# Kernel optimization log

Hardware: AMD Instinct MI355X
Metric: run time of the kernel (lower is better)

Reference implementation:

```python
import jax, jax.numpy as jnp
import numpy as np

B, S, E, D, M = 512, 64, 768, 256, 3  # batch, seq, encoder_dim, dim, num_modalities


def setup_inputs() -> dict:
    key = jax.random.key(0)
    ks = jax.random.split(key, 16)
    inp = {}
    for i in range(M):
        inp[f"latent{i}"] = jax.random.normal(ks[i], (B, S, E), dtype=jnp.float32)
        inp[f"Wp{i}"] = jax.random.normal(ks[3 + i], (D, E), dtype=jnp.float32) * (1.0 / np.sqrt(E))
        inp[f"bp{i}"] = jnp.zeros((D,), dtype=jnp.float32)
    inp["corr"] = jax.random.uniform(ks[7], (D, D), dtype=jnp.float32, minval=-0.1, maxval=0.1)
    F_in = 2 * D * (M - 1)  # 1024
    inp["Wb"] = jax.random.normal(ks[8], (64, F_in), dtype=jnp.float32) * (1.0 / np.sqrt(F_in))
    inp["bb"] = jnp.zeros((64,), dtype=jnp.float32)
    inp["gamma"] = jnp.ones((64,), dtype=jnp.float32)
    inp["beta"] = jnp.zeros((64,), dtype=jnp.float32)
    return inp


def _forward(latents, Wps, bps, corr, Wb, bb, gamma, beta):
    # project each modality: [B,S,E] -> [B,S,D]
    proj = [lat @ Wp.T + bp for lat, Wp, bp in zip(latents, Wps, bps)]
    anchor = proj[0]
    pairs = []
    for other in proj[1:]:
        # cc[b,i,j] = anchor[b,i,:] @ corr @ other[b,j,:]
        cc = jnp.einsum('bid,de,bje->bij', anchor, corr, other)
        a_att = jax.nn.softmax(cc, axis=1)   # softmax over anchor tokens
        o_att = jax.nn.softmax(cc, axis=2)   # softmax over other tokens (= softmax(cc^T, dim=1))
        att_anchor = jnp.einsum('bid,bij->bdj', anchor, a_att) + jnp.swapaxes(anchor, 1, 2)
        att_other = jnp.einsum('bjd,bij->bdi', other, o_att) + jnp.swapaxes(other, 1, 2)
        pairs.append(jnp.concatenate([att_anchor, att_other], axis=1))  # [B,2D,S]
    fused = jnp.concatenate(pairs, axis=1)          # [B, 2D(M-1), S]
    fused = jnp.swapaxes(fused, 1, 2)               # [B, S, 2D(M-1)]
    h = fused @ Wb.T + bb                           # [B, S, 64]
    mu = jnp.mean(h, axis=-1, keepdims=True)
    var = jnp.var(h, axis=-1, keepdims=True)
    h = (h - mu) / jnp.sqrt(var + 1e-5) * gamma + beta
    return jax.nn.relu(h)


def reference(latent0, latent1, latent2, Wp0, bp0, Wp1, bp1, Wp2, bp2, corr, Wb, bb, gamma, beta):
    return _forward([latent0, latent1, latent2], [Wp0, Wp1, Wp2], [bp0, bp1, bp2],
                    corr, Wb, bb, gamma, beta)
```

## Files before the change

### kernel.cpp

```cpp
#include <hip/hip_runtime.h>
#include <hip/hip_bf16.h>
#include <stdint.h>

#define Bsz 512
#define Ssz 64
#define Esz 768
#define Dsz 256
#define MROWS (Bsz * Ssz)
#define FIN 1024

typedef _Float16 f16;
typedef f16 f16x4 __attribute__((ext_vector_type(4)));
typedef f16 f16x8v __attribute__((ext_vector_type(8)));
typedef float f32x4 __attribute__((ext_vector_type(4)));

__device__ __forceinline__ void async_copy16(const void* g, void* l) {
    __builtin_amdgcn_global_load_lds((const __attribute__((address_space(1))) uint32_t*)g,
                                     (__attribute__((address_space(3))) uint32_t*)l, 16, 0, 0);
}

__global__ __launch_bounds__(256) void prep(const float* __restrict__ Wp0,
                                            const float* __restrict__ Wp1,
                                            const float* __restrict__ Wp2,
                                            const float* __restrict__ corr,
                                            const float* __restrict__ Wb,
                                            f16* __restrict__ Wph,
                                            f16* __restrict__ corrT,
                                            f16* __restrict__ Wbh) {
    const int t = blockIdx.x * 256 + threadIdx.x;
    if (t < 3 * 196608) {
        const int z = t / 196608, i = t % 196608;
        const float* W = (z == 0) ? Wp0 : (z == 1) ? Wp1 : Wp2;
        Wph[(size_t)z * 196608 + i] = (f16)W[i];
    }
    if (t < 65536) {
        const int d = t >> 8, e = t & 255;
        corrT[e * 256 + d] = (f16)corr[d * 256 + e];
        Wbh[t] = (f16)Wb[t];
    }
}

template <bool A_F16, bool BIAS>
__global__ __launch_bounds__(256) void mfma_gemm(
    const float* __restrict__ A32a, const float* __restrict__ A32b,
    const float* __restrict__ A32c, const f16* __restrict__ A16,
    const f16* __restrict__ Bh, const float* __restrict__ biasA,
    const float* __restrict__ biasB, const float* __restrict__ biasC,
    f16* __restrict__ Ch, int K) {
    constexpr int LDS_BYTES = A_F16 ? 32768 : 49152;
    __shared__ __align__(16) char smem[LDS_BYTES];
    float* Af32 = (float*)smem;
    f16* Af16 = (f16*)smem;
    f16* Bf = (f16*)(smem + (A_F16 ? 16384 : 32768));
    f16* Ce = (f16*)smem;

    const int tid = threadIdx.x;
    const int n0 = blockIdx.x * 128;
    const int m0 = blockIdx.y * 128;
    const int z = blockIdx.z;
    const float* A32 = (z == 0) ? A32a : (z == 1) ? A32b : A32c;
    const float* bias = (z == 0) ? biasA : (z == 1) ? biasB : biasC;
    const f16* Bz = Bh + (size_t)z * 256 * K;
    f16* Cz = Ch + (size_t)z * MROWS * 256;

    const int lane = tid & 63;
    const int w = tid >> 6;
    const int lr = lane & 15;
    const int lk = lane >> 4;
    const int ma = (w >> 1) * 4;
    const int nb = (w & 1) * 4;

    f32x4 acc[4][4];
#pragma unroll
    for (int i = 0; i < 4; i++)
#pragma unroll
        for (int j = 0; j < 4; j++) acc[i][j] = (f32x4){0.f, 0.f, 0.f, 0.f};

    for (int k0 = 0; k0 < K; k0 += 64) {
        __syncthreads();
#pragma unroll
        for (int i = 0; i < (A_F16 ? 4 : 8); i++) {
            const int Ub = (w * (A_F16 ? 4 : 8) + i) * 64;
            const int U = Ub + lane;
            if constexpr (A_F16) {
                const int row = U >> 3, u = (U & 7) ^ (row & 7);
                async_copy16(A16 + (size_t)(m0 + row) * K + k0 + u * 8, Af16 + (size_t)Ub * 8);
            } else {
                const int row = U >> 4, c = (U & 15) ^ (row & 15);
                async_copy16(A32 + (size_t)(m0 + row) * K + k0 + c * 4, Af32 + (size_t)Ub * 4);
            }
        }
#pragma unroll
        for (int i = 0; i < 4; i++) {
            const int Ub = (w * 4 + i) * 64;
            const int U = Ub + lane;
            const int row = U >> 3, u = (U & 7) ^ (row & 7);
            async_copy16(Bz + (size_t)(n0 + row) * K + k0 + u * 8, Bf + (size_t)Ub * 8);
        }
        __syncthreads();
#pragma unroll
        for (int kh = 0; kh < 2; kh++) {
            f16x8v af[4], bf[4];
#pragma unroll
            for (int i = 0; i < 4; i++) {
                const int row = (ma + i) * 16 + lr;
                if constexpr (A_F16) {
                    const int u = (kh * 4 + lk) ^ (row & 7);
                    af[i] = *(const f16x8v*)&Af16[(row * 8 + u) * 8];
                } else {
                    const int c = kh * 8 + lk * 2;
                    const float4 v1 = *(const float4*)&Af32[(row * 16 + (c ^ lr)) * 4];
                    const float4 v2 = *(const float4*)&Af32[(row * 16 + ((c + 1) ^ lr)) * 4];
                    f16x8v h;
                    h[0] = (f16)v1.x; h[1] = (f16)v1.y; h[2] = (f16)v1.z; h[3] = (f16)v1.w;
                    h[4] = (f16)v2.x; h[5] = (f16)v2.y; h[6] = (f16)v2.z; h[7] = (f16)v2.w;
                    af[i] = h;
                }
            }
#pragma unroll
            for (int j = 0; j < 4; j++) {
                const int row = (nb + j) * 16 + lr;
                const int u = (kh * 4 + lk) ^ (row & 7);
                bf[j] = *(const f16x8v*)&Bf[(row * 8 + u) * 8];
            }
#pragma unroll
            for (int i = 0; i < 4; i++)
#pragma unroll
                for (int j = 0; j < 4; j++)
                    acc[i][j] = __builtin_amdgcn_mfma_f32_16x16x32_f16(af[i], bf[j], acc[i][j], 0, 0, 0);
        }
    }

    __syncthreads();
    const int cr = lane & 15, qr = lane >> 4;
    const int mwl = (w >> 1) * 64;
    const int nwl = (w & 1) * 64;
#pragma unroll
    for (int i = 0; i < 4; i++) {
#pragma unroll
        for (int j = 0; j < 4; j++) {
            const int col = nwl + j * 16 + cr;
            const float bv = BIAS ? bias[n0 + col] : 0.f;
#pragma unroll
            for (int r = 0; r < 4; r++) {
                const int row = mwl + i * 16 + qr * 4 + r;
                Ce[row * 128 + col] = (f16)(acc[i][j][r] + bv);
            }
        }
    }
    __syncthreads();
#pragma unroll
    for (int r = 0; r < 8; r++) {
        const int f = r * 256 + tid;
        const int row = f >> 4, c16 = f & 15;
        uint4 v = *(const uint4*)&Ce[row * 128 + c16 * 8];
        *(uint4*)(Cz + (size_t)(m0 + row) * 256 + n0 + c16 * 8) = v;
    }
}

__global__ __launch_bounds__(256) void cc_softmax(const f16* __restrict__ ac,
                                                  const f16* __restrict__ proj1,
                                                  const f16* __restrict__ proj2,
                                                  f16* __restrict__ aT,
                                                  f16* __restrict__ oP) {
    const int b = blockIdx.x, q = blockIdx.y;
    const f16* __restrict__ A = ac + (size_t)b * Ssz * Dsz;
    const f16* __restrict__ Bp = (q ? proj2 : proj1) + (size_t)b * Ssz * Dsz;
    __shared__ float sc[64][65];
    __shared__ float cmax[64], csum[64], rmax[64], rsum[64];
    const int tid = threadIdx.x;
    const int lane = tid & 63, w = tid >> 6;
    const int lr = lane & 15;
    const int lk = lane >> 4;

    f32x4 acc[4];
#pragma unroll
    for (int j = 0; j < 4; j++) acc[j] = (f32x4){0.f, 0.f, 0.f, 0.f};

    const f16* __restrict__ Arow = A + (size_t)(w * 16 + lr) * Dsz + lk * 8;
    for (int ks = 0; ks < 8; ks++) {
        f16x8v af = *(const f16x8v*)(Arow + ks * 32);
        f16x8v bf[4];
#pragma unroll
        for (int j = 0; j < 4; j++)
            bf[j] = *(const f16x8v*)(Bp + (size_t)(j * 16 + lr) * Dsz + ks * 32 + lk * 8);
#pragma unroll
        for (int j = 0; j < 4; j++)
            acc[j] = __builtin_amdgcn_mfma_f32_16x16x32_f16(af, bf[j], acc[j], 0, 0, 0);
    }
#pragma unroll
    for (int j = 0; j < 4; j++)
#pragma unroll
        for (int r = 0; r < 4; r++) sc[w * 16 + lk * 4 + r][j * 16 + lr] = acc[j][r];
    __syncthreads();
    if (tid < 64) {
        const int j = tid;
        float m = -1e30f;
        for (int i = 0; i < 64; i++) m = fmaxf(m, sc[i][j]);
        float s = 0.f;
        for (int i = 0; i < 64; i++) s += __expf(sc[i][j] - m);
        cmax[j] = m;
        csum[j] = s;
    } else if (tid < 128) {
        const int i = tid - 64;
        float m = -1e30f;
        for (int j = 0; j < 64; j++) m = fmaxf(m, sc[i][j]);
        float s = 0.f;
        for (int j = 0; j < 64; j++) s += __expf(sc[i][j] - m);
        rmax[i] = m;
        rsum[i] = s;
    }
    __syncthreads();
    const int lid = tid & 63;
    const int grp = tid >> 6;
    f16* __restrict__ apT = aT + (size_t)(q * Bsz + b) * 4096;
    f16* __restrict__ opR = oP + (size_t)(q * Bsz + b) * 4096;
    for (int i = grp; i < 64; i += 4) {
        const float v = __expf(sc[i][lid] - rmax[i]) / rsum[i];
        opR[i * 64 + lid] = (f16)v;
    }
    for (int jj = grp; jj < 64; jj += 4) {
        const float v = __expf(sc[lid][jj] - cmax[jj]) / csum[jj];
        apT[jj * 64 + lid] = (f16)v;
    }
}

__global__ __launch_bounds__(256) void g_gemm(const f16* __restrict__ proj,
                                              const f16* __restrict__ Wbh,
                                              f16* __restrict__ G) {
    const int b = blockIdx.x;
    const int tid = threadIdx.x, lane = tid & 63, w = tid >> 6;
    const int q = w >> 1, part = w & 1;
    const int z = part ? (1 + q) : 0;
    const f16* __restrict__ X = proj + ((size_t)z * MROWS + b * 64) * 256;
    const f16* __restrict__ Wc = Wbh + q * 512 + part * 256;
    const int lr = lane & 15, lk = lane >> 4;

    f32x4 acc[4][4];
#pragma unroll
    for (int i = 0; i < 4; i++)
#pragma unroll
        for (int j = 0; j < 4; j++) acc[i][j] = (f32x4){0.f, 0.f, 0.f, 0.f};

    for (int ks = 0; ks < 8; ks++) {
        f16x8v af[4], bf[4];
#pragma unroll
        for (int mi = 0; mi < 4; mi++)
            af[mi] = *(const f16x8v*)(Wc + (size_t)(mi * 16 + lr) * FIN + ks * 32 + lk * 8);
#pragma unroll
        for (int nj = 0; nj < 4; nj++)
            bf[nj] = *(const f16x8v*)(X + (size_t)(nj * 16 + lr) * 256 + ks * 32 + lk * 8);
#pragma unroll
        for (int mi = 0; mi < 4; mi++)
#pragma unroll
            for (int nj = 0; nj < 4; nj++)
                acc[mi][nj] = __builtin_amdgcn_mfma_f32_16x16x32_f16(af[mi], bf[nj], acc[mi][nj], 0, 0, 0);
    }

    __shared__ __align__(16) f16 Gs[4][4096];
#pragma unroll
    for (int mi = 0; mi < 4; mi++)
#pragma unroll
        for (int nj = 0; nj < 4; nj++)
#pragma unroll
            for (int r = 0; r < 4; r++)
                Gs[w][(mi * 16 + lk * 4 + r) * 64 + nj * 16 + lr] = (f16)acc[mi][nj][r];
    __syncthreads();
#pragma unroll
    for (int r = 0; r < 8; r++) {
        const int u = r * 64 + lane;
        *(uint4*)(G + ((size_t)(b * 4 + w)) * 4096 + u * 8) = *(const uint4*)&Gs[w][u * 8];
    }
}

__global__ __launch_bounds__(256) void attn_ln(const f16* __restrict__ aT,
                                               const f16* __restrict__ oP,
                                               const f16* __restrict__ G,
                                               const float* __restrict__ bb,
                                               const float* __restrict__ gamma,
                                               const float* __restrict__ beta,
                                               float* __restrict__ out) {
    const int b = blockIdx.x;
    const int tid = threadIdx.x, lane = tid & 63, w = tid >> 6;
    const int lr = lane & 15, lk = lane >> 4;

    __shared__ __align__(16) f16 Gs[4][4096];
#pragma unroll
    for (int r = 0; r < 8; r++) {
        const int gu = r * 256 + tid;
        const int term = gu >> 9, u = gu & 511;
        const int o = u >> 3, tch = u & 7;
        uint4 v = *(const uint4*)(G + ((size_t)(b * 4 + term)) * 4096 + u * 8);
        const int su = o * 8 + (tch ^ (o & 7));
        *(uint4*)&Gs[term][su * 8] = v;
    }
    __syncthreads();

    f32x4 acc[4];
#pragma unroll
    for (int j = 0; j < 4; j++) acc[j] = (f32x4){0.f, 0.f, 0.f, 0.f};

#pragma unroll
    for (int term = 0; term < 4; term++) {
        const int q = term >> 1;
        const f16* __restrict__ Abase =
            ((term & 1) ? oP : aT) + ((size_t)(q * Bsz + b)) * 4096;
#pragma unroll
        for (int kh = 0; kh < 2; kh++) {
            f16x8v af = *(const f16x8v*)(Abase + (size_t)(w * 16 + lr) * 64 + kh * 32 + lk * 8);
#pragma unroll
            for (int jf = 0; jf < 4; jf++) {
                const int o = jf * 16 + lr;
                const int su = o * 8 + ((kh * 4 + lk) ^ (o & 7));
                f16x8v bf = *(const f16x8v*)&Gs[term][su * 8];
                acc[jf] = __builtin_amdgcn_mfma_f32_16x16x32_f16(af, bf, acc[jf], 0, 0, 0);
            }
        }
    }

    float bbv[4], gv[4], bv2[4];
#pragma unroll
    for (int jf = 0; jf < 4; jf++) {
        const int o = jf * 16 + lr;
        bbv[jf] = bb[o];
        gv[jf] = gamma[o];
        bv2[jf] = beta[o];
    }
#pragma unroll
    for (int r = 0; r < 4; r++) {
        const int s = w * 16 + lk * 4 + r;
        float h[4];
        float s1 = 0.f, s2 = 0.f;
#pragma unroll
        for (int jf = 0; jf < 4; jf++) {
            const int o = jf * 16 + lr;
            float resid = 0.f;
#pragma unroll
            for (int term = 0; term < 4; term++) {
                const int su = o * 8 + ((s >> 3) ^ (o & 7));
                resid += (float)Gs[term][su * 8 + (s & 7)];
            }
            h[jf] = acc[jf][r] + resid + bbv[jf];
            s1 += h[jf];
            s2 += h[jf] * h[jf];
        }
#pragma unroll
        for (int m = 1; m < 16; m <<= 1) {
            s1 += __shfl_xor(s1, m);
            s2 += __shfl_xor(s2, m);
        }
        const float mu = s1 * (1.f / 64.f);
        const float inv = rsqrtf(s2 * (1.f / 64.f) - mu * mu + 1e-5f);
#pragma unroll
        for (int jf = 0; jf < 4; jf++) {
            const float v = (h[jf] - mu) * inv * gv[jf] + bv2[jf];
            out[(size_t)(b * 64 + s) * 64 + jf * 16 + lr] = fmaxf(v, 0.f);
        }
    }
}

extern "C" void kernel_launch(void* const* d_in, const int* in_sizes, int n_in,
                              void* d_out, int out_size, void* d_ws, size_t ws_size,
                              hipStream_t stream) {
    const float* latent0 = (const float*)d_in[0];
    const float* Wp0 = (const float*)d_in[1];
    const float* bp0 = (const float*)d_in[2];
    const float* latent1 = (const float*)d_in[3];
    const float* Wp1 = (const float*)d_in[4];
    const float* bp1 = (const float*)d_in[5];
    const float* latent2 = (const float*)d_in[6];
    const float* Wp2 = (const float*)d_in[7];
    const float* bp2 = (const float*)d_in[8];
    const float* corr = (const float*)d_in[9];
    const float* Wb = (const float*)d_in[10];
    const float* bb = (const float*)d_in[11];
    const float* gamma = (const float*)d_in[12];
    const float* beta = (const float*)d_in[13];

    char* ws = (char*)d_ws;
    f16* proj_h = (f16*)ws;
    f16* ac_h = (f16*)(ws + 48ull * 1024 * 1024);
    f16* aT = (f16*)(ws + 64ull * 1024 * 1024);
    f16* oP = (f16*)(ws + 72ull * 1024 * 1024);
    f16* G = (f16*)(ws + 80ull * 1024 * 1024);
    f16* Wph = (f16*)(ws + 160ull * 1024 * 1024);
    f16* corrT = (f16*)(ws + 162ull * 1024 * 1024);
    f16* Wbh = (f16*)(ws + 162ull * 1024 * 1024 + 128ull * 1024);

    float* out = (float*)d_out;
    dim3 blk(256);

    prep<<<2304, blk, 0, stream>>>(Wp0, Wp1, Wp2, corr, Wb, Wph, corrT, Wbh);

    mfma_gemm<false, true><<<dim3(2, 256, 3), blk, 0, stream>>>(
        latent0, latent1, latent2, (const f16*)nullptr, Wph, bp0, bp1, bp2, proj_h, Esz);

    mfma_gemm<true, false><<<dim3(2, 256, 1), blk, 0, stream>>>(
        (const float*)nullptr, (const float*)nullptr, (const float*)nullptr, proj_h,
        corrT, (const float*)nullptr, (const float*)nullptr, (const float*)nullptr,
        ac_h, Dsz);

    const f16* proj1_h = proj_h + (size_t)MROWS * 256;
    const f16* proj2_h = proj_h + 2ull * MROWS * 256;

    cc_softmax<<<dim3(Bsz, 2), blk, 0, stream>>>(ac_h, proj1_h, proj2_h, aT, oP);

    g_gemm<<<Bsz, blk, 0, stream>>>(proj_h, Wbh, G);

    attn_ln<<<Bsz, blk, 0, stream>>>(aT, oP, G, bb, gamma, beta, out);

    (void)in_sizes; (void)n_in; (void)out_size; (void)ws_size;
}
```

Measured before the change: 396.6 us.

## Double-buffer GEMM loads, parallelize softmax stats, fuse G GEMM into tail

The projection GEMM now double-buffers its LDS tiles, issuing async loads for the next K slice while it computes on the current one, so each iteration waits on one barrier instead of two. The cc_softmax statistics are spread across all 256 threads using partial max and sum followed by a merge, replacing the old setup where only 128 threads did serial 64-element scans. The g_gemm kernel is folded into the attention/layernorm tail, which drops one launch and the round trip of G through global memory. In exchange, the GEMM uses twice as much LDS (96KB for the f32 variant), which can cut occupancy.

```diff
diff --git a/kernel.cpp b/kernel.cpp
--- a/kernel.cpp
+++ b/kernel.cpp
@@ -47,12 +47,9 @@
     const f16* __restrict__ Bh, const float* __restrict__ biasA,
     const float* __restrict__ biasB, const float* __restrict__ biasC,
     f16* __restrict__ Ch, int K) {
-    constexpr int LDS_BYTES = A_F16 ? 32768 : 49152;
-    __shared__ __align__(16) char smem[LDS_BYTES];
-    float* Af32 = (float*)smem;
-    f16* Af16 = (f16*)smem;
-    f16* Bf = (f16*)(smem + (A_F16 ? 16384 : 32768));
-    f16* Ce = (f16*)smem;
+    constexpr int ABYTES = A_F16 ? 16384 : 32768;
+    constexpr int BUF = ABYTES + 16384;
+    __shared__ __align__(16) char smem[2 * BUF];
 
     const int tid = threadIdx.x;
     const int n0 = blockIdx.x * 128;
@@ -76,18 +73,18 @@
 #pragma unroll
         for (int j = 0; j < 4; j++) acc[i][j] = (f32x4){0.f, 0.f, 0.f, 0.f};
 
-    for (int k0 = 0; k0 < K; k0 += 64) {
-        __syncthreads();
+    auto stage = [&](int buf, int k0) {
+        char* base = smem + buf * BUF;
 #pragma unroll
         for (int i = 0; i < (A_F16 ? 4 : 8); i++) {
             const int Ub = (w * (A_F16 ? 4 : 8) + i) * 64;
             const int U = Ub + lane;
             if constexpr (A_F16) {
                 const int row = U >> 3, u = (U & 7) ^ (row & 7);
-                async_copy16(A16 + (size_t)(m0 + row) * K + k0 + u * 8, Af16 + (size_t)Ub * 8);
+                async_copy16(A16 + (size_t)(m0 + row) * K + k0 + u * 8, base + Ub * 16);
             } else {
                 const int row = U >> 4, c = (U & 15) ^ (row & 15);
-                async_copy16(A32 + (size_t)(m0 + row) * K + k0 + c * 4, Af32 + (size_t)Ub * 4);
+                async_copy16(A32 + (size_t)(m0 + row) * K + k0 + c * 4, base + Ub * 16);
             }
         }
 #pragma unroll
@@ -95,9 +92,21 @@
             const int Ub = (w * 4 + i) * 64;
             const int U = Ub + lane;
             const int row = U >> 3, u = (U & 7) ^ (row & 7);
-            async_copy16(Bz + (size_t)(n0 + row) * K + k0 + u * 8, Bf + (size_t)Ub * 8);
-        }
-        __syncthreads();
+            async_copy16(Bz + (size_t)(n0 + row) * K + k0 + u * 8, base + ABYTES + Ub * 16);
+        }
+    };
+
+    stage(0, 0);
+    __syncthreads();
+    int cur = 0;
+    const int NT = K >> 6;
+    for (int t = 0; t < NT; t++) {
+        if (t + 1 < NT) stage(cur ^ 1, (t + 1) << 6);
+        __builtin_amdgcn_sched_barrier(0);
+        const char* base = smem + cur * BUF;
+        const f16* Af16L = (const f16*)base;
+        const float* Af32L = (const float*)base;
+        const f16* BfL = (const f16*)(base + ABYTES);
 #pragma unroll
         for (int kh = 0; kh < 2; kh++) {
             f16x8v af[4], bf[4];
@@ -106,11 +115,11 @@
                 const int row = (ma + i) * 16 + lr;
                 if constexpr (A_F16) {
                     const int u = (kh * 4 + lk) ^ (row & 7);
-                    af[i] = *(const f16x8v*)&Af16[(row * 8 + u) * 8];
+                    af[i] = *(const f16x8v*)&Af16L[(row * 8 + u) * 8];
                 } else {
                     const int c = kh * 8 + lk * 2;
-                    const float4 v1 = *(const float4*)&Af32[(row * 16 + (c ^ lr)) * 4];
-                    const float4 v2 = *(const float4*)&Af32[(row * 16 + ((c + 1) ^ lr)) * 4];
+                    const float4 v1 = *(const float4*)&Af32L[(row * 16 + (c ^ lr)) * 4];
+                    const float4 v2 = *(const float4*)&Af32L[(row * 16 + ((c + 1) ^ lr)) * 4];
                     f16x8v h;
                     h[0] = (f16)v1.x; h[1] = (f16)v1.y; h[2] = (f16)v1.z; h[3] = (f16)v1.w;
                     h[4] = (f16)v2.x; h[5] = (f16)v2.y; h[6] = (f16)v2.z; h[7] = (f16)v2.w;
@@ -121,7 +130,7 @@
             for (int j = 0; j < 4; j++) {
                 const int row = (nb + j) * 16 + lr;
                 const int u = (kh * 4 + lk) ^ (row & 7);
-                bf[j] = *(const f16x8v*)&Bf[(row * 8 + u) * 8];
+                bf[j] = *(const f16x8v*)&BfL[(row * 8 + u) * 8];
             }
 #pragma unroll
             for (int i = 0; i < 4; i++)
@@ -129,9 +138,11 @@
                 for (int j = 0; j < 4; j++)
                     acc[i][j] = __builtin_amdgcn_mfma_f32_16x16x32_f16(af[i], bf[j], acc[i][j], 0, 0, 0);
         }
-    }
-
-    __syncthreads();
+        __syncthreads();
+        cur ^= 1;
+    }
+
+    f16* Ce = (f16*)smem;
     const int cr = lane & 15, qr = lane >> 4;
     const int mwl = (w >> 1) * 64;
     const int nwl = (w & 1) * 64;
@@ -167,7 +178,8 @@
     const f16* __restrict__ A = ac + (size_t)b * Ssz * Dsz;
     const f16* __restrict__ Bp = (q ? proj2 : proj1) + (size_t)b * Ssz * Dsz;
     __shared__ float sc[64][65];
-    __shared__ float cmax[64], csum[64], rmax[64], rsum[64];
+    __shared__ float pm[4][64], ps[4][64], qm[4][64], qs[4][64];
+    __shared__ float CM[64], CI[64], RM[64], RI[64];
     const int tid = threadIdx.x;
     const int lane = tid & 63, w = tid >> 6;
     const int lr = lane & 15;
@@ -193,106 +205,95 @@
 #pragma unroll
         for (int r = 0; r < 4; r++) sc[w * 16 + lk * 4 + r][j * 16 + lr] = acc[j][r];
     __syncthreads();
-    if (tid < 64) {
-        const int j = tid;
-        float m = -1e30f;
-        for (int i = 0; i < 64; i++) m = fmaxf(m, sc[i][j]);
-        float s = 0.f;
-        for (int i = 0; i < 64; i++) s += __expf(sc[i][j] - m);
-        cmax[j] = m;
-        csum[j] = s;
-    } else if (tid < 128) {
-        const int i = tid - 64;
-        float m = -1e30f;
-        for (int j = 0; j < 64; j++) m = fmaxf(m, sc[i][j]);
-        float s = 0.f;
-        for (int j = 0; j < 64; j++) s += __expf(sc[i][j] - m);
-        rmax[i] = m;
-        rsum[i] = s;
-    }
-    __syncthreads();
-    const int lid = tid & 63;
-    const int grp = tid >> 6;
+
+    const int lid = tid & 63, qa = tid >> 6;
+    float m1 = -1e30f, m2 = -1e30f;
+#pragma unroll
+    for (int it = 0; it < 16; it++) {
+        m1 = fmaxf(m1, sc[qa * 16 + it][lid]);
+        m2 = fmaxf(m2, sc[lid][qa * 16 + it]);
+    }
+    float s1 = 0.f, s2 = 0.f;
+#pragma unroll
+    for (int it = 0; it < 16; it++) {
+        s1 += __expf(sc[qa * 16 + it][lid] - m1);
+        s2 += __expf(sc[lid][qa * 16 + it] - m2);
+    }
+    pm[qa][lid] = m1; ps[qa][lid] = s1;
+    qm[qa][lid] = m2; qs[qa][lid] = s2;
+    __syncthreads();
+    if (tid < 128) {
+        const int x = tid & 63;
+        const bool col = tid < 64;
+        float M = -1e30f;
+#pragma unroll
+        for (int u = 0; u < 4; u++) M = fmaxf(M, col ? pm[u][x] : qm[u][x]);
+        float S = 0.f;
+#pragma unroll
+        for (int u = 0; u < 4; u++)
+            S += (col ? ps[u][x] : qs[u][x]) * __expf((col ? pm[u][x] : qm[u][x]) - M);
+        if (col) { CM[x] = M; CI[x] = 1.f / S; }
+        else     { RM[x] = M; RI[x] = 1.f / S; }
+    }
+    __syncthreads();
     f16* __restrict__ apT = aT + (size_t)(q * Bsz + b) * 4096;
     f16* __restrict__ opR = oP + (size_t)(q * Bsz + b) * 4096;
-    for (int i = grp; i < 64; i += 4) {
-        const float v = __expf(sc[i][lid] - rmax[i]) / rsum[i];
-        opR[i * 64 + lid] = (f16)v;
-    }
-    for (int jj = grp; jj < 64; jj += 4) {
-        const float v = __expf(sc[lid][jj] - cmax[jj]) / csum[jj];
-        apT[jj * 64 + lid] = (f16)v;
-    }
-}
-
-__global__ __launch_bounds__(256) void g_gemm(const f16* __restrict__ proj,
-                                              const f16* __restrict__ Wbh,
-                                              f16* __restrict__ G) {
-    const int b = blockIdx.x;
-    const int tid = threadIdx.x, lane = tid & 63, w = tid >> 6;
-    const int q = w >> 1, part = w & 1;
-    const int z = part ? (1 + q) : 0;
-    const f16* __restrict__ X = proj + ((size_t)z * MROWS + b * 64) * 256;
-    const f16* __restrict__ Wc = Wbh + q * 512 + part * 256;
-    const int lr = lane & 15, lk = lane >> 4;
-
-    f32x4 acc[4][4];
-#pragma unroll
-    for (int i = 0; i < 4; i++)
-#pragma unroll
-        for (int j = 0; j < 4; j++) acc[i][j] = (f32x4){0.f, 0.f, 0.f, 0.f};
-
-    for (int ks = 0; ks < 8; ks++) {
-        f16x8v af[4], bf[4];
-#pragma unroll
-        for (int mi = 0; mi < 4; mi++)
-            af[mi] = *(const f16x8v*)(Wc + (size_t)(mi * 16 + lr) * FIN + ks * 32 + lk * 8);
-#pragma unroll
-        for (int nj = 0; nj < 4; nj++)
-            bf[nj] = *(const f16x8v*)(X + (size_t)(nj * 16 + lr) * 256 + ks * 32 + lk * 8);
-#pragma unroll
-        for (int mi = 0; mi < 4; mi++)
-#pragma unroll
-            for (int nj = 0; nj < 4; nj++)
-                acc[mi][nj] = __builtin_amdgcn_mfma_f32_16x16x32_f16(af[mi], bf[nj], acc[mi][nj], 0, 0, 0);
-    }
-
-    __shared__ __align__(16) f16 Gs[4][4096];
-#pragma unroll
-    for (int mi = 0; mi < 4; mi++)
-#pragma unroll
-        for (int nj = 0; nj < 4; nj++)
-#pragma unroll
-            for (int r = 0; r < 4; r++)
-                Gs[w][(mi * 16 + lk * 4 + r) * 64 + nj * 16 + lr] = (f16)acc[mi][nj][r];
-    __syncthreads();
-#pragma unroll
-    for (int r = 0; r < 8; r++) {
-        const int u = r * 64 + lane;
-        *(uint4*)(G + ((size_t)(b * 4 + w)) * 4096 + u * 8) = *(const uint4*)&Gs[w][u * 8];
-    }
-}
-
-__global__ __launch_bounds__(256) void attn_ln(const f16* __restrict__ aT,
-                                               const f16* __restrict__ oP,
-                                               const f16* __restrict__ G,
-                                               const float* __restrict__ bb,
-                                               const float* __restrict__ gamma,
-                                               const float* __restrict__ beta,
-                                               float* __restrict__ out) {
+#pragma unroll
+    for (int it = 0; it < 16; it++) {
+        const int i = qa * 16 + it;
+        opR[i * 64 + lid] = (f16)(__expf(sc[i][lid] - RM[i]) * RI[i]);
+        apT[i * 64 + lid] = (f16)(__expf(sc[lid][i] - CM[i]) * CI[i]);
+    }
+}
+
+__global__ __launch_bounds__(256) void fused_tail(const f16* __restrict__ proj,
+                                                  const f16* __restrict__ Wbh,
+                                                  const f16* __restrict__ aT,
+                                                  const f16* __restrict__ oP,
+                                                  const float* __restrict__ bb,
+                                                  const float* __restrict__ gamma,
+                                                  const float* __restrict__ beta,
+                                                  float* __restrict__ out) {
     const int b = blockIdx.x;
     const int tid = threadIdx.x, lane = tid & 63, w = tid >> 6;
     const int lr = lane & 15, lk = lane >> 4;
 
     __shared__ __align__(16) f16 Gs[4][4096];
-#pragma unroll
-    for (int r = 0; r < 8; r++) {
-        const int gu = r * 256 + tid;
-        const int term = gu >> 9, u = gu & 511;
-        const int o = u >> 3, tch = u & 7;
-        uint4 v = *(const uint4*)(G + ((size_t)(b * 4 + term)) * 4096 + u * 8);
-        const int su = o * 8 + (tch ^ (o & 7));
-        *(uint4*)&Gs[term][su * 8] = v;
+
+    {
+        const int q = w >> 1, part = w & 1;
+        const int z = part ? (1 + q) : 0;
+        const f16* __restrict__ X = proj + ((size_t)z * MROWS + b * 64) * 256;
+        const f16* __restrict__ Wc = Wbh + q * 512 + part * 256;
+        f32x4 gacc[4][4];
+#pragma unroll
+        for (int i = 0; i < 4; i++)
+#pragma unroll
+            for (int j = 0; j < 4; j++) gacc[i][j] = (f32x4){0.f, 0.f, 0.f, 0.f};
+        for (int ks = 0; ks < 8; ks++) {
+            f16x8v af[4], bf[4];
+#pragma unroll
+            for (int mi = 0; mi < 4; mi++)
+                af[mi] = *(const f16x8v*)(Wc + (size_t)(mi * 16 + lr) * FIN + ks * 32 + lk * 8);
+#pragma unroll
+            for (int nj = 0; nj < 4; nj++)
+                bf[nj] = *(const f16x8v*)(X + (size_t)(nj * 16 + lr) * 256 + ks * 32 + lk * 8);
+#pragma unroll
+            for (int mi = 0; mi < 4; mi++)
+#pragma unroll
+                for (int nj = 0; nj < 4; nj++)
+                    gacc[mi][nj] = __builtin_amdgcn_mfma_f32_16x16x32_f16(af[mi], bf[nj], gacc[mi][nj], 0, 0, 0);
+        }
+#pragma unroll
+        for (int mi = 0; mi < 4; mi++)
+#pragma unroll
+            for (int nj = 0; nj < 4; nj++)
+#pragma unroll
+                for (int r = 0; r < 4; r++) {
+                    const int o = mi * 16 + lk * 4 + r;
+                    const int t = nj * 16 + lr;
+                    Gs[w][(o * 8 + ((t >> 3) ^ (o & 7))) * 8 + (t & 7)] = (f16)gacc[mi][nj][r];
+                }
     }
     __syncthreads();
 
@@ -382,7 +383,6 @@
     f16* ac_h = (f16*)(ws + 48ull * 1024 * 1024);
     f16* aT = (f16*)(ws + 64ull * 1024 * 1024);
     f16* oP = (f16*)(ws + 72ull * 1024 * 1024);
-    f16* G = (f16*)(ws + 80ull * 1024 * 1024);
     f16* Wph = (f16*)(ws + 160ull * 1024 * 1024);
     f16* corrT = (f16*)(ws + 162ull * 1024 * 1024);
     f16* Wbh = (f16*)(ws + 162ull * 1024 * 1024 + 128ull * 1024);
@@ -405,9 +405,7 @@
 
     cc_softmax<<<dim3(Bsz, 2), blk, 0, stream>>>(ac_h, proj1_h, proj2_h, aT, oP);
 
-    g_gemm<<<Bsz, blk, 0, stream>>>(proj_h, Wbh, G);
-
-    attn_ln<<<Bsz, blk, 0, stream>>>(aT, oP, G, bb, gamma, beta, out);
+    fused_tail<<<Bsz, blk, 0, stream>>>(proj_h, Wbh, aT, oP, bb, gamma, beta, out);
 
     (void)in_sizes; (void)n_in; (void)out_size; (void)ws_size;
 }
```

Result: slower. 425.5 us (+7.3%).
